# Kernel tuning notes

Measured on AMD Instinct MI355X. Metric: run time of the kernel, lower is better.

## Reference

```python
import jax, jax.numpy as jnp
import numpy as np
import math

SCALES = (3, 5)
NUM_CLASSES = 10
D_NEIGHBOR = 64
NUM_GROUPS = 8  # min(8, d_neighbor)
GN_EPS = 1e-5


def setup_inputs() -> dict:
    key = jax.random.key(0)
    k0, k1, k2 = jax.random.split(key, 3)
    B, C, H, W = 8, NUM_CLASSES, 384, 384
    in_ch = 4 * len(SCALES)  # 8
    x = jax.random.normal(k0, (B, C, H, W), jnp.float32)
    W1 = jax.random.normal(k1, (D_NEIGHBOR, in_ch), jnp.float32) / np.sqrt(in_ch).astype(np.float32)
    b1 = jnp.zeros((D_NEIGHBOR,), jnp.float32)
    gn_w = jnp.ones((D_NEIGHBOR,), jnp.float32)
    gn_b = jnp.zeros((D_NEIGHBOR,), jnp.float32)
    W2 = jax.random.normal(k2, (D_NEIGHBOR, D_NEIGHBOR), jnp.float32) / np.sqrt(D_NEIGHBOR).astype(np.float32)
    b2 = jnp.zeros((D_NEIGHBOR,), jnp.float32)
    return {"x": x, "W1": W1, "b1": b1, "gn_w": gn_w, "gn_b": gn_b, "W2": W2, "b2": b2}


def _box_sum(P, k):
    """Depthwise k x k box-filter sum with replicate ('edge') padding."""
    pad = k // 2
    C = P.shape[1]
    Pp = jnp.pad(P, ((0, 0), (0, 0), (pad, pad), (pad, pad)), mode="edge")
    kern = jnp.ones((C, 1, k, k), P.dtype)
    return jax.lax.conv_general_dilated(
        Pp, kern, window_strides=(1, 1), padding="VALID",
        feature_group_count=C, dimension_numbers=("NCHW", "OIHW", "NCHW"))


def _neighbor_features(P):
    # P: (B, C, H, W) soft probabilities
    C = P.shape[1]
    log_C = math.log(NUM_CLASSES)
    feats = []
    for k in SCALES:
        K = float(k * k)
        S = _box_sum(P, k)                       # (B, C, H, W) window sums
        match = (P * (S - P)).sum(axis=1, keepdims=True) / (K - 1.0)
        maj = S.max(axis=1, keepdims=True) / K
        Pbar = S / K
        Pc = jnp.maximum(Pbar, 1e-8)
        ent = -(Pc * jnp.log(Pc)).sum(axis=1, keepdims=True)
        uni = 1.0 - ent / log_C
        S2 = _box_sum(P * P, k)
        var = (S2 / K - Pbar * Pbar).sum(axis=1, keepdims=True)
        feats += [match, maj, uni, var]
    return jnp.concatenate(feats, axis=1)        # (B, 4*len(SCALES), H, W)


def _group_norm(h, gn_w, gn_b):
    B, D, H, W = h.shape
    hg = h.reshape(B, NUM_GROUPS, D // NUM_GROUPS, H, W)
    mu = hg.mean(axis=(2, 3, 4), keepdims=True)
    var = hg.var(axis=(2, 3, 4), keepdims=True)
    hn = ((hg - mu) * jax.lax.rsqrt(var + GN_EPS)).reshape(B, D, H, W)
    return hn * gn_w[None, :, None, None] + gn_b[None, :, None, None]


def reference(x, W1, b1, gn_w, gn_b, W2, b2):
    P = jax.nn.softmax(x, axis=1)                       # (B, C, H, W)
    f = _neighbor_features(P)                           # (B, 8, H, W)
    h = jnp.einsum("bchw,dc->bdhw", f, W1) + b1[None, :, None, None]  # 1x1 conv
    h = _group_norm(h, gn_w, gn_b)
    h = jax.nn.gelu(h, approximate=False)               # torch default GELU (erf)
    out = jnp.einsum("bchw,dc->bdhw", h, W2) + b2[None, :, None, None]
    return out
```

## Files before the change

kernel.cpp:

```cpp
#include <hip/hip_runtime.h>
#include <math.h>

#define Bn 8
#define Cn 10
#define Hd 384
#define Wd 384
#define HW (Hd*Wd)
#define TX 32
#define TY 8
#define TLX 36
#define TLY 12
#define TSZ (TLX*TLY)
#define BLOCKS_PER_IMG 576
#define TILES_X 12

typedef __attribute__((ext_vector_type(8))) short s8v;
typedef __attribute__((ext_vector_type(4))) float f4v;

__device__ __forceinline__ unsigned short f2bf(float f) {
    unsigned u = __builtin_bit_cast(unsigned, f);
    u += 0x7fffu + ((u >> 16) & 1u);
    return (unsigned short)(u >> 16);
}

__device__ __forceinline__ float gelu_erf(float h) {
    float z  = 0.70710678118654752f * h;
    float az = fabsf(z);
    float t  = __builtin_amdgcn_rcpf(1.0f + 0.3275911f * az);
    float poly = ((((1.061405429f * t - 1.453152027f) * t + 1.421413741f) * t
                   - 0.284496736f) * t + 0.254829592f) * t;
    float e = __expf(-az * az);
    float erf_z = copysignf(1.0f - poly * e, z);
    return 0.5f * h * (1.0f + erf_z);
}

__global__ __launch_bounds__(256) void kA(const float* __restrict__ x,
                                          float* __restrict__ fout) {
    __shared__ float Pt[Cn * TSZ];
    const int bid = blockIdx.x;
    const int b   = bid / BLOCKS_PER_IMG;
    const int t   = bid % BLOCKS_PER_IMG;
    const int ty  = t / TILES_X, tx = t % TILES_X;
    const int x0  = tx * TX, y0 = ty * TY;
    const int tid = threadIdx.x;
    const float* xb = x + b * Cn * HW;

    for (int i = tid; i < TSZ; i += 256) {
        int ly = i / TLX, lx = i % TLX;
        int gy = y0 + ly - 2; gy = max(0, min(Hd - 1, gy));
        int gx = x0 + lx - 2; gx = max(0, min(Wd - 1, gx));
        const float* px = xb + gy * Wd + gx;
        float v[Cn];
        float m = -1e30f;
        #pragma unroll
        for (int c = 0; c < Cn; c++) { v[c] = px[c * HW]; m = fmaxf(m, v[c]); }
        float s = 0.f;
        #pragma unroll
        for (int c = 0; c < Cn; c++) { v[c] = __expf(v[c] - m); s += v[c]; }
        float inv = 1.0f / s;
        #pragma unroll
        for (int c = 0; c < Cn; c++) Pt[c * TSZ + i] = v[c] * inv;
    }
    __syncthreads();

    const int lx = tid % TX, ly = tid / TX;
    float match3 = 0.f, ent3 = 0.f, var3 = 0.f, maj3 = -1e30f;
    float match5 = 0.f, ent5 = 0.f, var5 = 0.f, maj5 = -1e30f;

    #pragma unroll 1
    for (int c = 0; c < Cn; c++) {
        const float* Pc = &Pt[c * TSZ + (ly + 2) * TLX + (lx + 2)];
        float S5 = 0.f, S3 = 0.f, Q5 = 0.f, Q3 = 0.f;
        #pragma unroll
        for (int dy = -2; dy <= 2; dy++) {
            #pragma unroll
            for (int dx = -2; dx <= 2; dx++) {
                float v = Pc[dy * TLX + dx];
                S5 += v; Q5 += v * v;
                if (dy >= -1 && dy <= 1 && dx >= -1 && dx <= 1) {
                    S3 += v; Q3 += v * v;
                }
            }
        }
        float pc = Pc[0];
        match3 += pc * (S3 - pc);
        match5 += pc * (S5 - pc);
        maj3 = fmaxf(maj3, S3);
        maj5 = fmaxf(maj5, S5);
        float q3 = fmaxf(S3 * (1.f / 9.f), 1e-8f);  ent3 -= q3 * __logf(q3);
        float q5 = fmaxf(S5 * (1.f / 25.f), 1e-8f); ent5 -= q5 * __logf(q5);
        float pb3 = S3 * (1.f / 9.f);  var3 += Q3 * (1.f / 9.f)  - pb3 * pb3;
        float pb5 = S5 * (1.f / 25.f); var5 += Q5 * (1.f / 25.f) - pb5 * pb5;
    }

    const float invlogC = 1.0f / 2.302585092994046f;
    float f0 = match3 * (1.f / 8.f);
    float f1 = maj3 * (1.f / 9.f);
    float f2 = 1.f - ent3 * invlogC;
    float f3 = var3;
    float f4 = match5 * (1.f / 24.f);
    float f5 = maj5 * (1.f / 25.f);
    float f6 = 1.f - ent5 * invlogC;
    float f7 = var5;

    int p = b * HW + (y0 + ly) * Wd + (x0 + lx);
    float4* o = (float4*)(fout + (size_t)p * 8);
    o[0] = make_float4(f0, f1, f2, f3);
    o[1] = make_float4(f4, f5, f6, f7);
}

__global__ __launch_bounds__(256) void kA2(const float* __restrict__ f,
                                           double* __restrict__ stats) {
    const int blk = blockIdx.x;
    const int b = blk / 9, sub = blk % 9;
    const int base = b * HW + sub * 16384;
    const int tid = threadIdx.x;

    float s[8];
    float q[36];
    #pragma unroll
    for (int i = 0; i < 8; i++) s[i] = 0.f;
    #pragma unroll
    for (int i = 0; i < 36; i++) q[i] = 0.f;

    for (int j = 0; j < 64; j++) {
        int p = base + j * 256 + tid;
        const float4* fv = (const float4*)(f + (size_t)p * 8);
        float4 a = fv[0], c4 = fv[1];
        float fl[8] = {a.x, a.y, a.z, a.w, c4.x, c4.y, c4.z, c4.w};
        int idx = 0;
        #pragma unroll
        for (int c = 0; c < 8; c++) {
            s[c] += fl[c];
            #pragma unroll
            for (int cp = c; cp < 8; cp++) { q[idx] += fl[c] * fl[cp]; idx++; }
        }
    }

    #pragma unroll
    for (int c = 0; c < 8; c++)
        for (int o = 32; o >= 1; o >>= 1) s[c] += __shfl_xor(s[c], o);
    #pragma unroll
    for (int i = 0; i < 36; i++)
        for (int o = 32; o >= 1; o >>= 1) q[i] += __shfl_xor(q[i], o);

    __shared__ float red[4][44];
    int lane = tid & 63, wv = tid >> 6;
    if (lane == 0) {
        #pragma unroll
        for (int c = 0; c < 8; c++) red[wv][c] = s[c];
        #pragma unroll
        for (int i = 0; i < 36; i++) red[wv][8 + i] = q[i];
    }
    __syncthreads();
    if (tid < 44) {
        float tot = red[0][tid] + red[1][tid] + red[2][tid] + red[3][tid];
        atomicAdd(&stats[b * 44 + tid], (double)tot);
    }
}

__global__ __launch_bounds__(512) void kB(const double* __restrict__ stats,
                                          const float* __restrict__ W1,
                                          const float* __restrict__ b1,
                                          const float* __restrict__ gnw,
                                          const float* __restrict__ gnb,
                                          float* __restrict__ ga,
                                          float* __restrict__ gb) {
    const int tid = threadIdx.x;
    const int b = tid >> 6, d = tid & 63;
    const double* st = stats + b * 44;
    const double invN = 1.0 / (double)HW;

    double m[8];
    #pragma unroll
    for (int c = 0; c < 8; c++) m[c] = st[c] * invN;
    double w[8];
    #pragma unroll
    for (int c = 0; c < 8; c++) w[c] = (double)W1[d * 8 + c];

    double wv = 0.0;
    #pragma unroll
    for (int c = 0; c < 8; c++) wv += w[c] * m[c];

    double quad = 0.0;
    int idx = 8;
    #pragma unroll
    for (int c = 0; c < 8; c++) {
        #pragma unroll
        for (int cp = c; cp < 8; cp++) {
            double e2 = st[idx] * invN; idx++;
            quad += (c == cp ? 1.0 : 2.0) * w[c] * w[cp] * e2;
        }
    }
    double bb  = (double)b1[d];
    double mu  = wv + bb;
    double eh2 = quad + 2.0 * bb * wv + bb * bb;

    double gm = mu, gq = eh2;
    #pragma unroll
    for (int o = 1; o < 8; o <<= 1) { gm += __shfl_xor(gm, o); gq += __shfl_xor(gq, o); }
    gm *= 0.125; gq *= 0.125;
    double var = gq - gm * gm;
    double rs  = rsqrt(var + 1e-5);

    float A  = (float)rs * gnw[d];
    float Bs = gnb[d] - (float)(gm * rs) * gnw[d];
    ga[tid] = A;
    gb[tid] = Bs;
}

__global__ __launch_bounds__(256) void kC2(const float* __restrict__ f,
                                           const float* __restrict__ W1,
                                           const float* __restrict__ b1,
                                           const float* __restrict__ W2,
                                           const float* __restrict__ b2,
                                           const float* __restrict__ ga,
                                           const float* __restrict__ gb,
                                           float* __restrict__ out) {
    __shared__ unsigned gl[256 * 33];
    const int b    = blockIdx.x / BLOCKS_PER_IMG;
    const int tile = blockIdx.x % BLOCKS_PER_IMG;
    const int pix0 = tile * 256;
    const int tid  = threadIdx.x;

    {
        const float4* fv = (const float4*)(f + ((size_t)(b * HW + pix0 + tid)) * 8);
        float4 A = fv[0], Bv = fv[1];
        float fl[8] = {A.x, A.y, A.z, A.w, Bv.x, Bv.y, Bv.z, Bv.w};
        const float* gaB = ga + b * 64;
        const float* gbB = gb + b * 64;
        unsigned* row = &gl[tid * 33];
        #pragma unroll
        for (int d2 = 0; d2 < 32; d2++) {
            float h0 = b1[2 * d2], h1 = b1[2 * d2 + 1];
            #pragma unroll
            for (int c = 0; c < 8; c++) {
                h0 += W1[(2 * d2) * 8 + c] * fl[c];
                h1 += W1[(2 * d2 + 1) * 8 + c] * fl[c];
            }
            h0 = h0 * gaB[2 * d2]     + gbB[2 * d2];
            h1 = h1 * gaB[2 * d2 + 1] + gbB[2 * d2 + 1];
            float g0 = gelu_erf(h0), g1 = gelu_erf(h1);
            row[d2] = (unsigned)f2bf(g0) | ((unsigned)f2bf(g1) << 16);
        }
    }
    __syncthreads();

    const int w    = tid >> 6;
    const int lane = tid & 63;
    const int quad = lane >> 4;
    const int col  = lane & 15;

    s8v afr[4][2];
    #pragma unroll
    for (int u = 0; u < 4; u++) {
        const float* wr = W2 + (size_t)(16 * u + col) * 64 + quad * 8;
        #pragma unroll
        for (int kc = 0; kc < 2; kc++) {
            const float4* w4 = (const float4*)(wr + 32 * kc);
            float4 x0 = w4[0], x1 = w4[1];
            union { unsigned short us[8]; s8v v; } cv;
            cv.us[0] = f2bf(x0.x); cv.us[1] = f2bf(x0.y);
            cv.us[2] = f2bf(x0.z); cv.us[3] = f2bf(x0.w);
            cv.us[4] = f2bf(x1.x); cv.us[5] = f2bf(x1.y);
            cv.us[6] = f2bf(x1.z); cv.us[7] = f2bf(x1.w);
            afr[u][kc] = cv.v;
        }
    }

    f4v acc[4][4];
    #pragma unroll
    for (int u = 0; u < 4; u++) {
        float b2r[4];
        #pragma unroll
        for (int r = 0; r < 4; r++) b2r[r] = b2[16 * u + quad * 4 + r];
        #pragma unroll
        for (int t = 0; t < 4; t++) {
            f4v a0; a0[0] = b2r[0]; a0[1] = b2r[1]; a0[2] = b2r[2]; a0[3] = b2r[3];
            acc[u][t] = a0;
        }
    }

    #pragma unroll
    for (int kc = 0; kc < 2; kc++) {
        s8v bfr[4];
        #pragma unroll
        for (int t = 0; t < 4; t++) {
            int px = 64 * w + 16 * t + col;
            const unsigned* r = &gl[px * 33 + kc * 16 + quad * 4];
            union { unsigned u[4]; s8v v; } cv;
            cv.u[0] = r[0]; cv.u[1] = r[1]; cv.u[2] = r[2]; cv.u[3] = r[3];
            bfr[t] = cv.v;
        }
        #pragma unroll
        for (int u = 0; u < 4; u++)
            #pragma unroll
            for (int t = 0; t < 4; t++)
                acc[u][t] = __builtin_amdgcn_mfma_f32_16x16x32_bf16(
                    afr[u][kc], bfr[t], acc[u][t], 0, 0, 0);
    }

    float* ob = out + (size_t)b * 64 * HW + pix0;
    #pragma unroll
    for (int u = 0; u < 4; u++) {
        #pragma unroll
        for (int t = 0; t < 4; t++) {
            int px = 64 * w + 16 * t + col;
            #pragma unroll
            for (int r = 0; r < 4; r++) {
                int e = 16 * u + quad * 4 + r;
                ob[(size_t)e * HW + px] = acc[u][t][r];
            }
        }
    }
}

extern "C" void kernel_launch(void* const* d_in, const int* in_sizes, int n_in,
                              void* d_out, int out_size, void* d_ws, size_t ws_size,
                              hipStream_t stream) {
    const float* x   = (const float*)d_in[0];
    const float* W1  = (const float*)d_in[1];
    const float* b1  = (const float*)d_in[2];
    const float* gnw = (const float*)d_in[3];
    const float* gnb = (const float*)d_in[4];
    const float* W2  = (const float*)d_in[5];
    const float* b2  = (const float*)d_in[6];
    float* out = (float*)d_out;

    char* ws = (char*)d_ws;
    const size_t FBYTES = (size_t)Bn * HW * 8 * sizeof(float);
    float*  fbuf  = (float*)ws;
    double* stats = (double*)(ws + FBYTES);
    float*  ga    = (float*)(ws + FBYTES + 8 * 44 * sizeof(double));
    float*  gbuf  = ga + Bn * 64;

    hipMemsetAsync(stats, 0, 8 * 44 * sizeof(double), stream);
    kA<<<Bn * BLOCKS_PER_IMG, 256, 0, stream>>>(x, fbuf);
    kA2<<<72, 256, 0, stream>>>(fbuf, stats);
    kB<<<1, 512, 0, stream>>>(stats, W1, b1, gnw, gnb, ga, gbuf);
    kC2<<<Bn * BLOCKS_PER_IMG, 256, 0, stream>>>(fbuf, W1, b1, W2, b2, ga, gbuf, out);
}
```

Before: 426.3 us.

## Restructure neighbor stencil layout, widen stats grid, vectorize output stores

The softmax tile in kA is stored pixel-major as three float4 per pixel, with the per-pixel sum of squares precomputed. The stencil then reads vectorized LDS and sums all classes at once, using an algebraic rewrite of match and variance. kA2 launches 576 blocks instead of 72 to spread the statistics reduction across more CUs, at the cost of more double atomics. kC2 swaps the MFMA operand order so each lane holds four consecutive pixels and can write float4 stores, and it uses a packed bf16 convert instruction.

```diff
diff --git a/kernel.cpp b/kernel.cpp
--- a/kernel.cpp
+++ b/kernel.cpp
@@ -36,14 +36,14 @@
 
 __global__ __launch_bounds__(256) void kA(const float* __restrict__ x,
                                           float* __restrict__ fout) {
-    __shared__ float Pt[Cn * TSZ];
+    __shared__ float4 Pt4[TSZ * 3];
     const int bid = blockIdx.x;
     const int b   = bid / BLOCKS_PER_IMG;
     const int t   = bid % BLOCKS_PER_IMG;
     const int ty  = t / TILES_X, tx = t % TILES_X;
     const int x0  = tx * TX, y0 = ty * TY;
     const int tid = threadIdx.x;
-    const float* xb = x + b * Cn * HW;
+    const float* xb = x + (size_t)b * Cn * HW;
 
     for (int i = tid; i < TSZ; i += 256) {
         int ly = i / TLX, lx = i % TLX;
@@ -58,50 +58,70 @@
         #pragma unroll
         for (int c = 0; c < Cn; c++) { v[c] = __expf(v[c] - m); s += v[c]; }
         float inv = 1.0f / s;
-        #pragma unroll
-        for (int c = 0; c < Cn; c++) Pt[c * TSZ + i] = v[c] * inv;
+        float U = 0.f;
+        #pragma unroll
+        for (int c = 0; c < Cn; c++) { v[c] *= inv; U += v[c] * v[c]; }
+        Pt4[i * 3 + 0] = make_float4(v[0], v[1], v[2], v[3]);
+        Pt4[i * 3 + 1] = make_float4(v[4], v[5], v[6], v[7]);
+        Pt4[i * 3 + 2] = make_float4(v[8], v[9], U, 0.f);
     }
     __syncthreads();
 
     const int lx = tid % TX, ly = tid / TX;
-    float match3 = 0.f, ent3 = 0.f, var3 = 0.f, maj3 = -1e30f;
-    float match5 = 0.f, ent5 = 0.f, var5 = 0.f, maj5 = -1e30f;
-
-    #pragma unroll 1
+    const float4* base = &Pt4[((ly + 2) * TLX + (lx + 2)) * 3];
+
+    float S5[Cn], S3[Cn], pc[Cn];
+    float U5 = 0.f, U3 = 0.f, Uc = 0.f;
+    #pragma unroll
+    for (int c = 0; c < Cn; c++) { S5[c] = 0.f; S3[c] = 0.f; }
+
+    #pragma unroll
+    for (int dy = -2; dy <= 2; dy++) {
+        #pragma unroll
+        for (int dx = -2; dx <= 2; dx++) {
+            const float4* rp = base + (dy * TLX + dx) * 3;
+            float4 r0 = rp[0], r1 = rp[1], r2 = rp[2];
+            float vv[Cn] = {r0.x, r0.y, r0.z, r0.w, r1.x, r1.y, r1.z, r1.w,
+                            r2.x, r2.y};
+            const bool inner = (dy >= -1 && dy <= 1 && dx >= -1 && dx <= 1);
+            #pragma unroll
+            for (int c = 0; c < Cn; c++) {
+                S5[c] += vv[c];
+                if (inner) S3[c] += vv[c];
+            }
+            U5 += r2.z;
+            if (inner) U3 += r2.z;
+            if (dy == 0 && dx == 0) {
+                #pragma unroll
+                for (int c = 0; c < Cn; c++) pc[c] = vv[c];
+                Uc = r2.z;
+            }
+        }
+    }
+
+    float dot3 = 0.f, dot5 = 0.f, maj3 = -1e30f, maj5 = -1e30f;
+    float ent3 = 0.f, ent5 = 0.f, sq3 = 0.f, sq5 = 0.f;
+    #pragma unroll
     for (int c = 0; c < Cn; c++) {
-        const float* Pc = &Pt[c * TSZ + (ly + 2) * TLX + (lx + 2)];
-        float S5 = 0.f, S3 = 0.f, Q5 = 0.f, Q3 = 0.f;
-        #pragma unroll
-        for (int dy = -2; dy <= 2; dy++) {
-            #pragma unroll
-            for (int dx = -2; dx <= 2; dx++) {
-                float v = Pc[dy * TLX + dx];
-                S5 += v; Q5 += v * v;
-                if (dy >= -1 && dy <= 1 && dx >= -1 && dx <= 1) {
-                    S3 += v; Q3 += v * v;
-                }
-            }
-        }
-        float pc = Pc[0];
-        match3 += pc * (S3 - pc);
-        match5 += pc * (S5 - pc);
-        maj3 = fmaxf(maj3, S3);
-        maj5 = fmaxf(maj5, S5);
-        float q3 = fmaxf(S3 * (1.f / 9.f), 1e-8f);  ent3 -= q3 * __logf(q3);
-        float q5 = fmaxf(S5 * (1.f / 25.f), 1e-8f); ent5 -= q5 * __logf(q5);
-        float pb3 = S3 * (1.f / 9.f);  var3 += Q3 * (1.f / 9.f)  - pb3 * pb3;
-        float pb5 = S5 * (1.f / 25.f); var5 += Q5 * (1.f / 25.f) - pb5 * pb5;
+        dot3 += pc[c] * S3[c];
+        dot5 += pc[c] * S5[c];
+        maj3 = fmaxf(maj3, S3[c]);
+        maj5 = fmaxf(maj5, S5[c]);
+        float q3 = fmaxf(S3[c] * (1.f / 9.f), 1e-8f);  ent3 -= q3 * __logf(q3);
+        float q5 = fmaxf(S5[c] * (1.f / 25.f), 1e-8f); ent5 -= q5 * __logf(q5);
+        float pb3 = S3[c] * (1.f / 9.f);  sq3 += pb3 * pb3;
+        float pb5 = S5[c] * (1.f / 25.f); sq5 += pb5 * pb5;
     }
 
     const float invlogC = 1.0f / 2.302585092994046f;
-    float f0 = match3 * (1.f / 8.f);
+    float f0 = (dot3 - Uc) * (1.f / 8.f);
     float f1 = maj3 * (1.f / 9.f);
     float f2 = 1.f - ent3 * invlogC;
-    float f3 = var3;
-    float f4 = match5 * (1.f / 24.f);
+    float f3 = U3 * (1.f / 9.f) - sq3;
+    float f4 = (dot5 - Uc) * (1.f / 24.f);
     float f5 = maj5 * (1.f / 25.f);
     float f6 = 1.f - ent5 * invlogC;
-    float f7 = var5;
+    float f7 = U5 * (1.f / 25.f) - sq5;
 
     int p = b * HW + (y0 + ly) * Wd + (x0 + lx);
     float4* o = (float4*)(fout + (size_t)p * 8);
@@ -112,8 +132,8 @@
 __global__ __launch_bounds__(256) void kA2(const float* __restrict__ f,
                                            double* __restrict__ stats) {
     const int blk = blockIdx.x;
-    const int b = blk / 9, sub = blk % 9;
-    const int base = b * HW + sub * 16384;
+    const int b = blk / 72, sub = blk % 72;
+    const int base = b * HW + sub * 2048;
     const int tid = threadIdx.x;
 
     float s[8];
@@ -123,7 +143,7 @@
     #pragma unroll
     for (int i = 0; i < 36; i++) q[i] = 0.f;
 
-    for (int j = 0; j < 64; j++) {
+    for (int j = 0; j < 8; j++) {
         int p = base + j * 256 + tid;
         const float4* fv = (const float4*)(f + (size_t)p * 8);
         float4 a = fv[0], c4 = fv[1];
@@ -241,7 +261,9 @@
             h0 = h0 * gaB[2 * d2]     + gbB[2 * d2];
             h1 = h1 * gaB[2 * d2 + 1] + gbB[2 * d2 + 1];
             float g0 = gelu_erf(h0), g1 = gelu_erf(h1);
-            row[d2] = (unsigned)f2bf(g0) | ((unsigned)f2bf(g1) << 16);
+            unsigned pk;
+            asm("v_cvt_pk_bf16_f32 %0, %1, %2" : "=v"(pk) : "v"(g0), "v"(g1));
+            row[d2] = pk;
         }
     }
     __syncthreads();
@@ -251,7 +273,7 @@
     const int quad = lane >> 4;
     const int col  = lane & 15;
 
-    s8v afr[4][2];
+    s8v wfr[4][2];
     #pragma unroll
     for (int u = 0; u < 4; u++) {
         const float* wr = W2 + (size_t)(16 * u + col) * 64 + quad * 8;
@@ -264,53 +286,49 @@
             cv.us[2] = f2bf(x0.z); cv.us[3] = f2bf(x0.w);
             cv.us[4] = f2bf(x1.x); cv.us[5] = f2bf(x1.y);
             cv.us[6] = f2bf(x1.z); cv.us[7] = f2bf(x1.w);
-            afr[u][kc] = cv.v;
-        }
-    }
-
-    f4v acc[4][4];
+            wfr[u][kc] = cv.v;
+        }
+    }
+
+    f4v acc2[4][4];
     #pragma unroll
     for (int u = 0; u < 4; u++) {
-        float b2r[4];
-        #pragma unroll
-        for (int r = 0; r < 4; r++) b2r[r] = b2[16 * u + quad * 4 + r];
+        float bv = b2[16 * u + col];
         #pragma unroll
         for (int t = 0; t < 4; t++) {
-            f4v a0; a0[0] = b2r[0]; a0[1] = b2r[1]; a0[2] = b2r[2]; a0[3] = b2r[3];
-            acc[u][t] = a0;
+            f4v a0; a0[0] = bv; a0[1] = bv; a0[2] = bv; a0[3] = bv;
+            acc2[t][u] = a0;
         }
     }
 
     #pragma unroll
     for (int kc = 0; kc < 2; kc++) {
-        s8v bfr[4];
+        s8v gfr[4];
         #pragma unroll
         for (int t = 0; t < 4; t++) {
             int px = 64 * w + 16 * t + col;
             const unsigned* r = &gl[px * 33 + kc * 16 + quad * 4];
-            union { unsigned u[4]; s8v v; } cv;
-            cv.u[0] = r[0]; cv.u[1] = r[1]; cv.u[2] = r[2]; cv.u[3] = r[3];
-            bfr[t] = cv.v;
+            union { unsigned u4[4]; s8v v; } cv;
+            cv.u4[0] = r[0]; cv.u4[1] = r[1]; cv.u4[2] = r[2]; cv.u4[3] = r[3];
+            gfr[t] = cv.v;
         }
         #pragma unroll
         for (int u = 0; u < 4; u++)
             #pragma unroll
             for (int t = 0; t < 4; t++)
-                acc[u][t] = __builtin_amdgcn_mfma_f32_16x16x32_bf16(
-                    afr[u][kc], bfr[t], acc[u][t], 0, 0, 0);
+                acc2[t][u] = __builtin_amdgcn_mfma_f32_16x16x32_bf16(
+                    gfr[t], wfr[u][kc], acc2[t][u], 0, 0, 0);
     }
 
     float* ob = out + (size_t)b * 64 * HW + pix0;
     #pragma unroll
     for (int u = 0; u < 4; u++) {
+        float* oe = ob + (size_t)(16 * u + col) * HW + 64 * w + quad * 4;
         #pragma unroll
         for (int t = 0; t < 4; t++) {
-            int px = 64 * w + 16 * t + col;
-            #pragma unroll
-            for (int r = 0; r < 4; r++) {
-                int e = 16 * u + quad * 4 + r;
-                ob[(size_t)e * HW + px] = acc[u][t][r];
-            }
+            float4 sv = make_float4(acc2[t][u][0], acc2[t][u][1],
+                                    acc2[t][u][2], acc2[t][u][3]);
+            *(float4*)(oe + 16 * t) = sv;
         }
     }
 }
@@ -336,7 +354,7 @@
 
     hipMemsetAsync(stats, 0, 8 * 44 * sizeof(double), stream);
     kA<<<Bn * BLOCKS_PER_IMG, 256, 0, stream>>>(x, fbuf);
-    kA2<<<72, 256, 0, stream>>>(fbuf, stats);
+    kA2<<<576, 256, 0, stream>>>(fbuf, stats);
     kB<<<1, 512, 0, stream>>>(stats, W1, b1, gnw, gnb, ga, gbuf);
     kC2<<<Bn * BLOCKS_PER_IMG, 256, 0, stream>>>(fbuf, W1, b1, W2, b2, ga, gbuf, out);
 }
```

Result: slower. 446.3 us (+4.7%).
